# Kernel tuning notes

Measured on AMD Instinct MI355X. Metric: run time of the kernel, lower is better.

## Reference

```python
import jax, jax.numpy as jnp
import numpy as np

N = 262144      # number of 3D points
D = 128         # in_channels
NCLS = 20       # classes
M = 10          # num_prototype
EPS = 0.05      # sinkhorn epsilon
ITERS = 3       # sinkhorn iterations
GAMMA = 0.99    # EMA momentum
LN_EPS = 1e-5

def layer_norm(x, g, b):
    mu = jnp.mean(x, axis=-1, keepdims=True)
    v = jnp.mean((x - mu) ** 2, axis=-1, keepdims=True)
    return (x - mu) / jnp.sqrt(v + LN_EPS) * g + b

def l2n(x):
    # F.normalize(p=2, dim=-1) with eps=1e-12
    return x / jnp.clip(jnp.linalg.norm(x, axis=-1, keepdims=True), 1e-12)

def setup_inputs() -> dict:
    key = jax.random.key(0)
    k1, k2, k3 = jax.random.split(key, 3)
    return {
        "feature3d": jax.random.normal(k1, (N, D), dtype=jnp.float32),
        "gt_seg": jax.random.randint(k2, (N,), 0, NCLS, dtype=jnp.int32),
        "prototypes": jax.random.normal(k3, (NCLS, M, D), dtype=jnp.float32),
        "feat_gamma": jnp.ones((D,), jnp.float32),
        "feat_beta": jnp.zeros((D,), jnp.float32),
        "mask_gamma": jnp.ones((NCLS,), jnp.float32),
        "mask_beta": jnp.zeros((NCLS,), jnp.float32),
    }

def reference(feature3d, gt_seg, prototypes, feat_gamma, feat_beta, mask_gamma, mask_beta):
    _c = l2n(layer_norm(feature3d, feat_gamma, feat_beta))            # [N,D]
    protos = l2n(prototypes)                                          # [K,M,D]
    masks = jnp.einsum('nd,kmd->nmk', _c, protos)                     # [N,M,K]
    out_seg = layer_norm(jnp.max(masks, axis=1), mask_gamma, mask_beta)  # [N,K]

    # ---- prototype_learning ----
    pred = jnp.argmax(out_seg, axis=-1)
    correct = (gt_seg == pred).astype(_c.dtype)                       # [N]
    proto_logits = _c @ protos.reshape(-1, D).T                       # [N,K*M]

    sel = jax.nn.one_hot(gt_seg, NCLS, dtype=_c.dtype)                # [N,K]
    # masked per-class sinkhorn, vectorized across all 20 classes
    L = jnp.exp(jnp.transpose(masks, (2, 1, 0)) / EPS) * sel.T[:, None, :]  # [K,M,N]
    B = jnp.sum(sel, axis=0)                                          # [K] points per class
    s = jnp.sum(L, axis=(1, 2), keepdims=True)
    L = L / jnp.where(s > 0, s, 1.0)
    Bsafe = jnp.where(B > 0, B, 1.0)[:, None, None]
    for _ in range(ITERS):
        rs = jnp.sum(L, axis=2, keepdims=True)                        # per-prototype row sum
        L = L / (jnp.where(rs > 0, rs, 1.0) * M)
        cs = jnp.sum(L, axis=1, keepdims=True)                        # per-point col sum
        L = L / jnp.where(cs > 0, cs, 1.0) / Bsafe
    L = L * B[:, None, None]

    idx = jnp.argmax(L, axis=1)                                       # [K,N] hard assignment
    q = jax.nn.one_hot(idx, M, dtype=_c.dtype)                        # [K,N,M] (one_hot(argmax))

    w = sel.T * correct[None, :]                                      # [K,N] class-k AND correct
    m_q = q * w[:, :, None]                                           # [K,N,M]
    f = jnp.einsum('knm,nd->kmd', m_q, _c * correct[:, None])         # [K,M,D]
    ncount = jnp.sum(m_q, axis=1)                                     # [K,M]
    fn = l2n(f)
    upd = GAMMA * protos + (1.0 - GAMMA) * fn                         # momentum_update
    new_protos = l2n(jnp.where(ncount[..., None] > 0, upd, protos))   # [K,M,D]

    idx_pp = idx[gt_seg, jnp.arange(N)]                               # per-point proto index
    proto_target = (idx_pp + M * gt_seg).astype(jnp.float32)          # [N]
    return out_seg, proto_logits, proto_target, new_protos
```

## Files before the change

### kernel.cpp

```cpp
#include <hip/hip_runtime.h>
#include <hip/hip_bf16.h>

#define NPTS 262144
#define DIM  128
#define KC   20
#define MP   10
#define LNEPS 1e-5f
#define EPSI  0.05f
#define CCAP  65536

typedef _Float16 half8 __attribute__((ext_vector_type(8)));
typedef float f32x4 __attribute__((ext_vector_type(4)));
typedef float fv4 __attribute__((ext_vector_type(4)));

union H8U4 { half8 h; uint4 u; };

#define WS_PN     0
#define WS_PHI    25600
#define WS_PLO    39936
#define WS_F      54272
#define WS_NCOUNT 79872
#define WS_CCNT   80072
#define WS_UH     80080
#define WS_SK     80680
#define WS_BC     80700
#define WS_PSB    80720
#define WS_PR     244560
#define WS_EXPV   449360
#define WS_CIDX   3595088

#define EPIT 212

#define MFMA_(b_, a_, c_) __builtin_amdgcn_mfma_f32_16x16x32_f16(b_, a_, c_, 0, 0, 0)

__device__ __forceinline__ half8 lds_h8(const uint4* p) {
    return *reinterpret_cast<const half8*>(p);
}

__device__ __forceinline__ void gload_lds16(const uint4* g, uint4* l) {
    __builtin_amdgcn_global_load_lds(
        (const __attribute__((address_space(1))) void*)(g),
        (__attribute__((address_space(3))) void*)(l), 16, 0, 0);
}

__device__ __forceinline__ void nt_store4(float* p, float x, float y, float z, float w) {
    fv4 v = {x, y, z, w};
    __builtin_nontemporal_store(v, (fv4*)p);
}

__global__ __launch_bounds__(64) void k_norm_protos(
    const float* __restrict__ pr, float* __restrict__ pn,
    _Float16* __restrict__ phi, _Float16* __restrict__ plo)
{
    int j = blockIdx.x, l = threadIdx.x;
    const int jm = j & 15;
    const int s1 = l >> 3,       swz1 = (((s1 ^ jm) << 3) | (l & 7));
    const int s2 = 8 + (l >> 3), swz2 = (((s2 ^ jm) << 3) | (l & 7));
    if (j < 200) {
        float x0 = pr[(size_t)j*128 + l], x1 = pr[(size_t)j*128 + 64 + l];
        float ss = x0*x0 + x1*x1;
        #pragma unroll
        for (int off = 32; off > 0; off >>= 1) ss += __shfl_xor(ss, off);
        float dn = fmaxf(sqrtf(ss), 1e-12f);
        float y0 = x0/dn, y1 = x1/dn;
        pn[(size_t)j*128 + l]      = y0;
        pn[(size_t)j*128 + 64 + l] = y1;
        _Float16 h0 = (_Float16)y0, h1 = (_Float16)y1;
        phi[(size_t)j*128 + swz1] = h0;
        phi[(size_t)j*128 + swz2] = h1;
        plo[(size_t)j*128 + swz1] = (_Float16)(y0 - (float)h0);
        plo[(size_t)j*128 + swz2] = (_Float16)(y1 - (float)h1);
    } else {
        phi[(size_t)j*128 + swz1] = (_Float16)0.f;  phi[(size_t)j*128 + swz2] = (_Float16)0.f;
        plo[(size_t)j*128 + swz1] = (_Float16)0.f;  plo[(size_t)j*128 + swz2] = (_Float16)0.f;
    }
}

__global__ __launch_bounds__(256, 3) void k_main(
    const float* __restrict__ feat, const int* __restrict__ gt,
    const _Float16* __restrict__ phi, const _Float16* __restrict__ plo,
    const float* __restrict__ fg, const float* __restrict__ fb,
    const float* __restrict__ mg, const float* __restrict__ mb,
    float* __restrict__ out_seg, float* __restrict__ plog,
    float* __restrict__ expv, float* __restrict__ psb,
    int* __restrict__ cidx, int* __restrict__ ccnt)
{
    __shared__ __align__(16) char ldsb[33280];
    uint4* bbuf = (uint4*)ldsb;
    float* epi  = (float*)ldsb;
    float* osg  = (float*)(ldsb + 27136);
    float* exs  = (float*)(ldsb + 29696);
    float* sumS = (float*)(ldsb + 31232);
    int*   gtS  = (int*)  (ldsb + 31488);
    float* part = (float*)(ldsb + 31744);

    const int t = threadIdx.x, blk = blockIdx.x;
    const int w = t >> 6, lane = t & 63;
    const int l15 = lane & 15, l4 = lane >> 4;
    const int pbase = blk * 64;

    const uint4* phi4 = (const uint4*)phi;
    const uint4* plo4 = (const uint4*)plo;

#define STAGE_B(S, BI) do { \
        const uint4* gh = phi4 + (size_t)(S)*512 + t; \
        const uint4* gl = plo4 + (size_t)(S)*512 + t; \
        uint4* dh = bbuf + (BI)*1024 + w*64; \
        uint4* dl = bbuf + (BI)*1024 + 512 + w*64; \
        gload_lds16(gh,       dh); \
        gload_lds16(gh + 256, dh + 256); \
        gload_lds16(gl,       dl); \
        gload_lds16(gl + 256, dl + 256); \
    } while (0)

    STAGE_B(0, 0);

    const float4* gfeat = (const float4*)feat;
    float4 A[4][2];
    {
        size_t rb = (size_t)(pbase + w*16 + l15) * 32;
        #pragma unroll
        for (int kst = 0; kst < 4; ++kst)
            #pragma unroll
            for (int h = 0; h < 2; ++h)
                A[kst][h] = gfeat[rb + kst*8 + l4*2 + h];
    }
    float4 G[4][2], Bb[4][2];
    {
        const float4* fg4 = (const float4*)fg;
        const float4* fb4 = (const float4*)fb;
        #pragma unroll
        for (int kst = 0; kst < 4; ++kst)
            #pragma unroll
            for (int h = 0; h < 2; ++h) {
                G[kst][h]  = fg4[kst*8 + l4*2 + h];
                Bb[kst][h] = fb4[kst*8 + l4*2 + h];
            }
    }

    half8 fah[4], fal[4];
    {
        float s0 = 0.f;
        #pragma unroll
        for (int kst = 0; kst < 4; ++kst)
            #pragma unroll
            for (int h = 0; h < 2; ++h) {
                float4 v = A[kst][h];
                s0 += v.x + v.y + v.z + v.w;
            }
        s0 += __shfl_xor(s0, 16); s0 += __shfl_xor(s0, 32);
        float mean = s0 * (1.f/128.f);
        float s1 = 0.f;
        #pragma unroll
        for (int kst = 0; kst < 4; ++kst)
            #pragma unroll
            for (int h = 0; h < 2; ++h) {
                float4 v = A[kst][h];
                float a = v.x-mean, b = v.y-mean, c = v.z-mean, d = v.w-mean;
                s1 += a*a + b*b + c*c + d*d;
            }
        s1 += __shfl_xor(s1, 16); s1 += __shfl_xor(s1, 32);
        float rstd = rsqrtf(s1 * (1.f/128.f) + LNEPS);
        float s2 = 0.f;
        #pragma unroll
        for (int kst = 0; kst < 4; ++kst)
            #pragma unroll
            for (int h = 0; h < 2; ++h) {
                float4 v = A[kst][h];
                float4 g = G[kst][h], bb = Bb[kst][h];
                v.x = (v.x-mean)*rstd*g.x + bb.x;
                v.y = (v.y-mean)*rstd*g.y + bb.y;
                v.z = (v.z-mean)*rstd*g.z + bb.z;
                v.w = (v.w-mean)*rstd*g.w + bb.w;
                A[kst][h] = v;
                s2 += v.x*v.x + v.y*v.y + v.z*v.z + v.w*v.w;
            }
        s2 += __shfl_xor(s2, 16); s2 += __shfl_xor(s2, 32);
        float rl2 = 1.f / fmaxf(sqrtf(s2), 1e-12f);
        #pragma unroll
        for (int kst = 0; kst < 4; ++kst) {
            float4 va = A[kst][0], vb = A[kst][1];
            va.x*=rl2; va.y*=rl2; va.z*=rl2; va.w*=rl2;
            vb.x*=rl2; vb.y*=rl2; vb.z*=rl2; vb.w*=rl2;
            H8U4 h, lo;
            h.h[0]=(_Float16)va.x; h.h[1]=(_Float16)va.y; h.h[2]=(_Float16)va.z; h.h[3]=(_Float16)va.w;
            h.h[4]=(_Float16)vb.x; h.h[5]=(_Float16)vb.y; h.h[6]=(_Float16)vb.z; h.h[7]=(_Float16)vb.w;
            lo.h[0]=(_Float16)(va.x-(float)h.h[0]); lo.h[1]=(_Float16)(va.y-(float)h.h[1]);
            lo.h[2]=(_Float16)(va.z-(float)h.h[2]); lo.h[3]=(_Float16)(va.w-(float)h.h[3]);
            lo.h[4]=(_Float16)(vb.x-(float)h.h[4]); lo.h[5]=(_Float16)(vb.y-(float)h.h[5]);
            lo.h[6]=(_Float16)(vb.z-(float)h.h[6]); lo.h[7]=(_Float16)(vb.w-(float)h.h[7]);
            fah[kst] = h.h;
            fal[kst] = lo.h;
        }
    }

    f32x4 acc[13];
    #pragma unroll
    for (int nt = 0; nt < 13; ++nt)
        acc[nt] = (f32x4){0.f,0.f,0.f,0.f};

    __syncthreads();

    #pragma unroll
    for (int s = 0; s < 7; ++s) {
        if (s < 6) STAGE_B(s + 1, (s + 1) & 1);
        const uint4* bb = bbuf + (s & 1)*1024;
        if (s < 6) {
            #pragma unroll
            for (int kst = 0; kst < 4; ++kst) {
                const int slz = (kst*4 + l4) ^ l15;
                half8 b0h = lds_h8(bb + l15*16 + slz);
                half8 b0l = lds_h8(bb + 512 + l15*16 + slz);
                half8 b1h = lds_h8(bb + (16+l15)*16 + slz);
                half8 b1l = lds_h8(bb + 512 + (16+l15)*16 + slz);
                acc[2*s]   = MFMA_(b0h, fah[kst], acc[2*s]);
                acc[2*s+1] = MFMA_(b1h, fah[kst], acc[2*s+1]);
                acc[2*s]   = MFMA_(b0h, fal[kst], acc[2*s]);
                acc[2*s+1] = MFMA_(b1h, fal[kst], acc[2*s+1]);
                acc[2*s]   = MFMA_(b0l, fah[kst], acc[2*s]);
                acc[2*s+1] = MFMA_(b1l, fah[kst], acc[2*s+1]);
                acc[2*s]   = MFMA_(b0l, fal[kst], acc[2*s]);
                acc[2*s+1] = MFMA_(b1l, fal[kst], acc[2*s+1]);
            }
        } else {
            #pragma unroll
            for (int kst = 0; kst < 4; ++kst) {
                const int slz = (kst*4 + l4) ^ l15;
                half8 b0h = lds_h8(bb + l15*16 + slz);
                half8 b0l = lds_h8(bb + 512 + l15*16 + slz);
                acc[12] = MFMA_(b0h, fah[kst], acc[12]);
                acc[12] = MFMA_(b0h, fal[kst], acc[12]);
                acc[12] = MFMA_(b0l, fah[kst], acc[12]);
                acc[12] = MFMA_(b0l, fal[kst], acc[12]);
            }
        }
        __syncthreads();
    }

    #pragma unroll 1
    for (int p = 0; p < 2; ++p) {
        if ((w >> 1) == p) {
            int row = (w & 1)*16 + l15;
            #pragma unroll
            for (int nt = 0; nt < 13; ++nt)
                if (nt < 12 || l4 < 2) {
                    float4 sv;
                    sv.x = acc[nt][0]; sv.y = acc[nt][1];
                    sv.z = acc[nt][2]; sv.w = acc[nt][3];
                    *reinterpret_cast<float4*>(&epi[row*EPIT + nt*16 + l4*4]) = sv;
                }
        }
        __syncthreads();
        {
            float* pdst = plog + (size_t)(pbase + p*32)*200;
            #pragma unroll
            for (int it = 0; it < 7; ++it) {
                int f = it*256 + t;
                if (f < 1600) {
                    int row = f / 50, c4 = f - row*50;
                    const float* sp = &epi[row*EPIT + c4*4];
                    nt_store4(&pdst[(size_t)f*4], sp[0], sp[1], sp[2], sp[3]);
                }
            }
        }
        if (t < 128) {
            const int q = t >> 2, sub = t & 3;
            const int n = pbase + p*32 + q;
            float ml[5];
            #pragma unroll
            for (int kk = 0; kk < 5; ++kk) {
                int k = sub*5 + kk;
                float mx = epi[q*EPIT + k*10];
                #pragma unroll
                for (int m = 1; m < 10; ++m) mx = fmaxf(mx, epi[q*EPIT + k*10 + m]);
                ml[kk] = mx;
            }
            float s0 = ml[0]+ml[1]+ml[2]+ml[3]+ml[4];
            s0 += __shfl_xor(s0,1); s0 += __shfl_xor(s0,2);
            float mean = s0 / 20.f;
            float s1 = 0.f;
            #pragma unroll
            for (int kk = 0; kk < 5; ++kk) { float d = ml[kk]-mean; s1 += d*d; }
            s1 += __shfl_xor(s1,1); s1 += __shfl_xor(s1,2);
            float rstd = rsqrtf(s1 / 20.f + LNEPS);
            float bv = -1e30f; int bk = 0;
            #pragma unroll
            for (int kk = 0; kk < 5; ++kk) {
                int k = sub*5 + kk;
                float y = (ml[kk]-mean)*rstd*mg[k] + mb[k];
                osg[q*20 + k] = y;
                if (y > bv) { bv = y; bk = k; }
            }
            #pragma unroll
            for (int off = 1; off <= 2; off <<= 1) {
                float ov = __shfl_xor(bv, off);
                int   ok = __shfl_xor(bk, off);
                if (ov > bv || (ov == bv && ok < bk)) { bv = ov; bk = ok; }
            }
            int g = gt[n];
            if (sub == 0) {
                if (bk == g) {
                    int slot = atomicAdd(ccnt, 1);
                    if (slot < CCAP) cidx[slot] = n;
                }
                float se = 0.f;
                #pragma unroll
                for (int m = 0; m < 10; ++m) {
                    float e = expf(epi[q*EPIT + g*10 + m] / EPSI);
                    exs[q*12 + m] = e;
                    se += e;
                }
                exs[q*12 + 10] = 0.f;
                exs[q*12 + 11] = 0.f;
                sumS[p*32 + q] = se;
                gtS[p*32 + q]  = g;
            }
        }
        __syncthreads();
        if (t < 160) {
            const float* sp = &osg[t*4];
            nt_store4(&out_seg[(size_t)(pbase + p*32)*20 + t*4], sp[0], sp[1], sp[2], sp[3]);
        } else if (t < 256 && (t - 160) < 96)
            *reinterpret_cast<float4*>(&expv[(size_t)(pbase + p*32)*12 + (t-160)*4])
                = *reinterpret_cast<const float4*>(&exs[(t-160)*4]);
        __syncthreads();
    }

    if (t < 160) {
        int c = t >> 3, o = t & 7;
        float cnt = 0.f, sm = 0.f;
        for (int i = o*8; i < o*8 + 8; ++i)
            if (gtS[i] == c) { cnt += 1.f; sm += sumS[i]; }
        part[t] = cnt; part[160 + t] = sm;
    }
    __syncthreads();
    if (t < 20) {
        float cnt = 0.f, sm = 0.f;
        #pragma unroll
        for (int o = 0; o < 8; ++o) { cnt += part[t*8+o]; sm += part[160 + t*8+o]; }
        psb[(size_t)t*4096 + blk]      = cnt;
        psb[(size_t)(20+t)*4096 + blk] = sm;
    }
#undef STAGE_B
}

__global__ __launch_bounds__(256) void k_reduce_sB(
    const float* __restrict__ psb, float* __restrict__ sk, float* __restrict__ Bc)
{
    __shared__ float red[256];
    int t = threadIdx.x, rrow = blockIdx.x;
    float s = 0.f;
    #pragma unroll
    for (int i = 0; i < 16; ++i) s += psb[(size_t)rrow*4096 + i*256 + t];
    red[t] = s; __syncthreads();
    for (int off = 128; off > 0; off >>= 1) { if (t < off) red[t] += red[t+off]; __syncthreads(); }
    if (t == 0) { if (rrow < 20) Bc[rrow] = red[0]; else sk[rrow-20] = red[0]; }
}

__global__ __launch_bounds__(256) void k_row(int iter,
    const int* __restrict__ gt, const float* __restrict__ expv,
    const float* __restrict__ uh, const float* __restrict__ sk,
    const float* __restrict__ Bc, float* __restrict__ pr)
{
    __shared__ float prodS[2560];
    __shared__ int gtS[256];
    int t = threadIdx.x, b = blockIdx.x;
    int n = b*256 + t;
    int g = gt[n];
    float e[10];
    {
        const float4* e4 = (const float4*)(expv + (size_t)n*12);
        float4 ea = e4[0], eb = e4[1], ec = e4[2];
        e[0]=ea.x; e[1]=ea.y; e[2]=ea.z; e[3]=ea.w;
        e[4]=eb.x; e[5]=eb.y; e[6]=eb.z; e[7]=eb.w;
        e[8]=ec.x; e[9]=ec.y;
    }
    float skg = sk[g];
    float v = (skg > 0.f) ? 1.f/skg : 1.f;
    float B = Bc[g];
    float Bs = (B > 0.f) ? B : 1.f;
    for (int c = 1; c < iter; ++c) {
        const float* uc = uh + (c-1)*200 + g*10;
        float sc = 0.f;
        #pragma unroll
        for (int m = 0; m < 10; ++m) sc += e[m]*uc[m];
        v = (sc > 0.f) ? 1.f/(Bs*sc) : v/Bs;
    }
    #pragma unroll
    for (int m = 0; m < 10; ++m) prodS[t*10+m] = e[m]*v;
    gtS[t] = g;
    __syncthreads();
    if (t < 200) {
        int kk = t / 10, mm = t % 10;
        float acc = 0.f;
        for (int i = 0; i < 256; ++i)
            if (gtS[i] == kk) acc += prodS[i*10+mm];
        pr[(size_t)t*1024 + b] = acc;
    }
}

__global__ __launch_bounds__(256) void k_reduce_u(int iter,
    const float* __restrict__ pr, float* __restrict__ uh)
{
    __shared__ float red[256];
    int t = threadIdx.x, j = blockIdx.x;
    float s = 0.f;
    #pragma unroll
    for (int i = 0; i < 4; ++i) s += pr[(size_t)j*1024 + i*256 + t];
    red[t] = s; __syncthreads();
    for (int off = 128; off > 0; off >>= 1) { if (t < off) red[t] += red[t+off]; __syncthreads(); }
    if (t == 0) {
        float S = red[0];
        float uprev = (iter == 1) ? 1.f : uh[(iter-2)*200 + j];
        uh[(iter-1)*200 + j] = (S > 0.f) ? 1.f/(10.f*S) : uprev*0.1f;
    }
}

__global__ __launch_bounds__(256) void k_post(
    const int* __restrict__ gt, const float* __restrict__ expv,
    const float* __restrict__ u,
    const int* __restrict__ cidx, const int* __restrict__ ccnt,
    const float* __restrict__ feat, const float* __restrict__ fg,
    const float* __restrict__ fb,
    float* __restrict__ ptarget, float* __restrict__ facc,
    float* __restrict__ ncount)
{
    int t = threadIdx.x;
    {
        int n = blockIdx.x*256 + t;
        int g = gt[n];
        const float* uk = u + g*10;
        float bv = -1e30f; int idx = 0;
        #pragma unroll
        for (int m = 0; m < 10; ++m) {
            float pm = expv[(size_t)n*12 + m] * uk[m];
            if (pm > bv) { bv = pm; idx = m; }
        }
        ptarget[n] = (float)(idx + 10*g);
    }
    int wid = blockIdx.x*4 + (t >> 6);
    int lane = t & 63;
    int cnt = *ccnt; if (cnt > CCAP) cnt = CCAP;
    for (int i = wid; i < cnt; i += 4096) {
        int n = cidx[i];
        float x0 = feat[(size_t)n*128 + lane], x1 = feat[(size_t)n*128 + 64 + lane];
        float s = x0 + x1;
        #pragma unroll
        for (int off = 32; off > 0; off >>= 1) s += __shfl_xor(s, off);
        float mean = s * (1.f/128.f);
        float d0 = x0 - mean, d1 = x1 - mean;
        float s2 = d0*d0 + d1*d1;
        #pragma unroll
        for (int off = 32; off > 0; off >>= 1) s2 += __shfl_xor(s2, off);
        float rstd = rsqrtf(s2 * (1.f/128.f) + LNEPS);
        float y0 = d0*rstd*fg[lane] + fb[lane];
        float y1 = d1*rstd*fg[64+lane] + fb[64+lane];
        float s3 = y0*y0 + y1*y1;
        #pragma unroll
        for (int off = 32; off > 0; off >>= 1) s3 += __shfl_xor(s3, off);
        float rl2 = 1.f / fmaxf(sqrtf(s3), 1e-12f);
        float c0 = y0*rl2, c1 = y1*rl2;
        int g = gt[n];
        const float* uk = u + g*10;
        float bv = -1e30f; int idx = 0;
        #pragma unroll
        for (int m = 0; m < 10; ++m) {
            float pm = expv[(size_t)n*12 + m] * uk[m];
            if (pm > bv) { bv = pm; idx = m; }
        }
        float* frow = facc + (size_t)(g*10+idx)*128;
        atomicAdd(&frow[lane], c0);
        atomicAdd(&frow[64+lane], c1);
        if (lane == 0) atomicAdd(&ncount[g*10+idx], 1.f);
    }
}

__global__ __launch_bounds__(64) void k_proto_update(
    const float* __restrict__ facc, const float* __restrict__ ncount,
    const float* __restrict__ pn, float* __restrict__ outp)
{
    const float OMG = (float)(1.0 - 0.99);
    int j = blockIdx.x, l = threadIdx.x;
    float f0 = facc[(size_t)j*128+l], f1 = facc[(size_t)j*128+64+l];
    float ss = f0*f0 + f1*f1;
    #pragma unroll
    for (int off = 32; off > 0; off >>= 1) ss += __shfl_xor(ss, off);
    float fl2 = fmaxf(sqrtf(ss), 1e-12f);
    float fn0 = f0/fl2, fn1 = f1/fl2;
    float p0 = pn[(size_t)j*128+l], p1 = pn[(size_t)j*128+64+l];
    float u0 = 0.99f*p0 + OMG*fn0, u1 = 0.99f*p1 + OMG*fn1;
    bool ok = ncount[j] > 0.f;
    float s0 = ok ? u0 : p0, s1 = ok ? u1 : p1;
    float ss2 = s0*s0 + s1*s1;
    #pragma unroll
    for (int off = 32; off > 0; off >>= 1) ss2 += __shfl_xor(ss2, off);
    float l2 = fmaxf(sqrtf(ss2), 1e-12f);
    outp[(size_t)j*128+l]      = s0/l2;
    outp[(size_t)j*128+64+l]   = s1/l2;
}

extern "C" void kernel_launch(void* const* d_in, const int* in_sizes, int n_in,
                              void* d_out, int out_size, void* d_ws, size_t ws_size,
                              hipStream_t stream)
{
    const float* feat   = (const float*)d_in[0];
    const int*   gt     = (const int*)  d_in[1];
    const float* protos = (const float*)d_in[2];
    const float* fg     = (const float*)d_in[3];
    const float* fb     = (const float*)d_in[4];
    const float* mg     = (const float*)d_in[5];
    const float* mb     = (const float*)d_in[6];

    float* out      = (float*)d_out;
    float* out_seg  = out;
    float* plog     = out + (size_t)NPTS*20;
    float* ptarget  = out + (size_t)NPTS*220;
    float* newp     = out + (size_t)NPTS*221;

    float* ws   = (float*)d_ws;
    float* pn   = ws + WS_PN;
    _Float16* phi = (_Float16*)(ws + WS_PHI);
    _Float16* plo = (_Float16*)(ws + WS_PLO);
    float* facc = ws + WS_F;
    float* ncnt = ws + WS_NCOUNT;
    int*   ccnt = (int*)(ws + WS_CCNT);
    float* uh   = ws + WS_UH;
    float* sk   = ws + WS_SK;
    float* Bc   = ws + WS_BC;
    float* psb  = ws + WS_PSB;
    float* pr   = ws + WS_PR;
    float* expv = ws + WS_EXPV;
    int*   cidx = (int*)(ws + WS_CIDX);

    hipMemsetAsync(facc, 0, (25600 + 200 + 8)*sizeof(float), stream);
    hipLaunchKernelGGL(k_norm_protos, dim3(224), dim3(64), 0, stream, protos, pn, phi, plo);
    hipLaunchKernelGGL(k_main, dim3(4096), dim3(256), 0, stream,
                       feat, gt, phi, plo, fg, fb, mg, mb, out_seg, plog, expv, psb,
                       cidx, ccnt);
    hipLaunchKernelGGL(k_reduce_sB, dim3(40), dim3(256), 0, stream, psb, sk, Bc);
    for (int it = 1; it <= 3; ++it) {
        hipLaunchKernelGGL(k_row, dim3(1024), dim3(256), 0, stream, it, gt, expv, uh, sk, Bc, pr);
        hipLaunchKernelGGL(k_reduce_u, dim3(200), dim3(256), 0, stream, it, pr, uh);
    }
    hipLaunchKernelGGL(k_post, dim3(1024), dim3(256), 0, stream,
                       gt, expv, uh + 400, cidx, ccnt, feat, fg, fb, ptarget, facc, ncnt);
    hipLaunchKernelGGL(k_proto_update, dim3(200), dim3(64), 0, stream, facc, ncnt, pn, newp);
}
```

Before: 246.3 us.

## Fold first Sinkhorn row-sum pass into main kernel and pack exp values

The main kernel now accumulates per-block, per-(class,prototype) sums of the exp values and writes them as partials. A merged reduction kernel derives the point counts, the class sums and the first Sinkhorn row scaling directly from these partials, so the first k_row/k_reduce_u pass over all points is no longer launched. The exp buffer is also packed to 10 floats per point instead of 12 to cut bandwidth, and k_main's launch bound rises to 4 blocks per SIMD. In exchange the main kernel does extra LDS scans per block and writes a larger partial array, and the reduction kernel now runs serially over 11 rows per class.

```diff
diff --git a/kernel.cpp b/kernel.cpp
--- a/kernel.cpp
+++ b/kernel.cpp
@@ -25,9 +25,9 @@
 #define WS_SK     80680
 #define WS_BC     80700
 #define WS_PSB    80720
-#define WS_PR     244560
-#define WS_EXPV   449360
-#define WS_CIDX   3595088
+#define WS_EP     162640
+#define WS_EXPV   981840
+#define WS_CIDX   3603280
 
 #define EPIT 212
 
@@ -76,13 +76,13 @@
     }
 }
 
-__global__ __launch_bounds__(256, 3) void k_main(
+__global__ __launch_bounds__(256, 4) void k_main(
     const float* __restrict__ feat, const int* __restrict__ gt,
     const _Float16* __restrict__ phi, const _Float16* __restrict__ plo,
     const float* __restrict__ fg, const float* __restrict__ fb,
     const float* __restrict__ mg, const float* __restrict__ mb,
     float* __restrict__ out_seg, float* __restrict__ plog,
-    float* __restrict__ expv, float* __restrict__ psb,
+    float* __restrict__ expv, float* __restrict__ psb, float* __restrict__ ep,
     int* __restrict__ cidx, int* __restrict__ ccnt)
 {
     __shared__ __align__(16) char ldsb[33280];
@@ -90,9 +90,8 @@
     float* epi  = (float*)ldsb;
     float* osg  = (float*)(ldsb + 27136);
     float* exs  = (float*)(ldsb + 29696);
-    float* sumS = (float*)(ldsb + 31232);
-    int*   gtS  = (int*)  (ldsb + 31488);
-    float* part = (float*)(ldsb + 31744);
+    int*   gtS  = (int*)  (ldsb + 30976);
+    float* part = (float*)(ldsb + 31232);
 
     const int t = threadIdx.x, blk = blockIdx.x;
     const int w = t >> 6, lane = t & 63;
@@ -237,6 +236,7 @@
         __syncthreads();
     }
 
+    float eacc = 0.f;
     #pragma unroll 1
     for (int p = 0; p < 2; ++p) {
         if ((w >> 1) == p) {
@@ -303,58 +303,74 @@
                     int slot = atomicAdd(ccnt, 1);
                     if (slot < CCAP) cidx[slot] = n;
                 }
-                float se = 0.f;
                 #pragma unroll
-                for (int m = 0; m < 10; ++m) {
-                    float e = expf(epi[q*EPIT + g*10 + m] / EPSI);
-                    exs[q*12 + m] = e;
-                    se += e;
-                }
-                exs[q*12 + 10] = 0.f;
-                exs[q*12 + 11] = 0.f;
-                sumS[p*32 + q] = se;
-                gtS[p*32 + q]  = g;
+                for (int m = 0; m < 10; ++m)
+                    exs[q*10 + m] = expf(epi[q*EPIT + g*10 + m] / EPSI);
+                gtS[p*32 + q] = g;
             }
         }
         __syncthreads();
         if (t < 160) {
             const float* sp = &osg[t*4];
             nt_store4(&out_seg[(size_t)(pbase + p*32)*20 + t*4], sp[0], sp[1], sp[2], sp[3]);
-        } else if (t < 256 && (t - 160) < 96)
-            *reinterpret_cast<float4*>(&expv[(size_t)(pbase + p*32)*12 + (t-160)*4])
-                = *reinterpret_cast<const float4*>(&exs[(t-160)*4]);
+        } else if (t < 240) {
+            int f = t - 160;
+            *reinterpret_cast<float4*>(&expv[(size_t)(pbase + p*32)*10 + f*4])
+                = *reinterpret_cast<const float4*>(&exs[f*4]);
+        }
+        if (t < 200) {
+            int kk = t / 10, mm = t - kk*10;
+            #pragma unroll 4
+            for (int i = 0; i < 32; ++i)
+                if (gtS[p*32 + i] == kk) eacc += exs[i*10 + mm];
+        }
         __syncthreads();
     }
 
     if (t < 160) {
         int c = t >> 3, o = t & 7;
-        float cnt = 0.f, sm = 0.f;
+        float cnt = 0.f;
         for (int i = o*8; i < o*8 + 8; ++i)
-            if (gtS[i] == c) { cnt += 1.f; sm += sumS[i]; }
-        part[t] = cnt; part[160 + t] = sm;
+            if (gtS[i] == c) cnt += 1.f;
+        part[t] = cnt;
     }
     __syncthreads();
     if (t < 20) {
-        float cnt = 0.f, sm = 0.f;
-        #pragma unroll
-        for (int o = 0; o < 8; ++o) { cnt += part[t*8+o]; sm += part[160 + t*8+o]; }
-        psb[(size_t)t*4096 + blk]      = cnt;
-        psb[(size_t)(20+t)*4096 + blk] = sm;
-    }
+        float cnt = 0.f;
+        #pragma unroll
+        for (int o = 0; o < 8; ++o) cnt += part[t*8+o];
+        psb[(size_t)t*4096 + blk] = cnt;
+    }
+    if (t < 200) ep[(size_t)t*4096 + blk] = eacc;
 #undef STAGE_B
 }
 
-__global__ __launch_bounds__(256) void k_reduce_sB(
-    const float* __restrict__ psb, float* __restrict__ sk, float* __restrict__ Bc)
+__global__ __launch_bounds__(256) void k_red1(
+    const float* __restrict__ psb, const float* __restrict__ ep,
+    float* __restrict__ Bc, float* __restrict__ sk, float* __restrict__ uh)
 {
     __shared__ float red[256];
-    int t = threadIdx.x, rrow = blockIdx.x;
-    float s = 0.f;
-    #pragma unroll
-    for (int i = 0; i < 16; ++i) s += psb[(size_t)rrow*4096 + i*256 + t];
-    red[t] = s; __syncthreads();
-    for (int off = 128; off > 0; off >>= 1) { if (t < off) red[t] += red[t+off]; __syncthreads(); }
-    if (t == 0) { if (rrow < 20) Bc[rrow] = red[0]; else sk[rrow-20] = red[0]; }
+    __shared__ float rs[11];
+    int t = threadIdx.x, k = blockIdx.x;
+    for (int r = 0; r < 11; ++r) {
+        const float* src = (r == 0) ? (psb + (size_t)k*4096)
+                                    : (ep + (size_t)(k*10 + r - 1)*4096);
+        float s = 0.f;
+        #pragma unroll
+        for (int i = 0; i < 16; ++i) s += src[i*256 + t];
+        red[t] = s; __syncthreads();
+        for (int off = 128; off > 0; off >>= 1) { if (t < off) red[t] += red[t+off]; __syncthreads(); }
+        if (t == 0) rs[r] = red[0];
+        __syncthreads();
+    }
+    if (t < 16) {
+        float S = rs[1]+rs[2]+rs[3]+rs[4]+rs[5]+rs[6]+rs[7]+rs[8]+rs[9]+rs[10];
+        if (t == 0) { Bc[k] = rs[0]; sk[k] = S; }
+        if (t < 10) {
+            float r1 = (S > 0.f) ? rs[1+t] / S : rs[1+t];
+            uh[k*10 + t] = (r1 > 0.f) ? 1.f/(10.f*r1) : 0.1f;
+        }
+    }
 }
 
 __global__ __launch_bounds__(256) void k_row(int iter,
@@ -369,11 +385,10 @@
     int g = gt[n];
     float e[10];
     {
-        const float4* e4 = (const float4*)(expv + (size_t)n*12);
-        float4 ea = e4[0], eb = e4[1], ec = e4[2];
-        e[0]=ea.x; e[1]=ea.y; e[2]=ea.z; e[3]=ea.w;
-        e[4]=eb.x; e[5]=eb.y; e[6]=eb.z; e[7]=eb.w;
-        e[8]=ec.x; e[9]=ec.y;
+        const float2* e2 = (const float2*)(expv + (size_t)n*10);
+        float2 a0=e2[0], a1=e2[1], a2=e2[2], a3=e2[3], a4=e2[4];
+        e[0]=a0.x; e[1]=a0.y; e[2]=a1.x; e[3]=a1.y; e[4]=a2.x;
+        e[5]=a2.y; e[6]=a3.x; e[7]=a3.y; e[8]=a4.x; e[9]=a4.y;
     }
     float skg = sk[g];
     float v = (skg > 0.f) ? 1.f/skg : 1.f;
@@ -411,7 +426,7 @@
     for (int off = 128; off > 0; off >>= 1) { if (t < off) red[t] += red[t+off]; __syncthreads(); }
     if (t == 0) {
         float S = red[0];
-        float uprev = (iter == 1) ? 1.f : uh[(iter-2)*200 + j];
+        float uprev = uh[(iter-2)*200 + j];
         uh[(iter-1)*200 + j] = (S > 0.f) ? 1.f/(10.f*S) : uprev*0.1f;
     }
 }
@@ -430,11 +445,14 @@
         int n = blockIdx.x*256 + t;
         int g = gt[n];
         const float* uk = u + g*10;
+        const float2* e2 = (const float2*)(expv + (size_t)n*10);
         float bv = -1e30f; int idx = 0;
         #pragma unroll
-        for (int m = 0; m < 10; ++m) {
-            float pm = expv[(size_t)n*12 + m] * uk[m];
-            if (pm > bv) { bv = pm; idx = m; }
+        for (int m2 = 0; m2 < 5; ++m2) {
+            float2 ev = e2[m2];
+            float p0 = ev.x * uk[m2*2], p1 = ev.y * uk[m2*2+1];
+            if (p0 > bv) { bv = p0; idx = m2*2; }
+            if (p1 > bv) { bv = p1; idx = m2*2+1; }
         }
         ptarget[n] = (float)(idx + 10*g);
     }
@@ -462,11 +480,14 @@
         float c0 = y0*rl2, c1 = y1*rl2;
         int g = gt[n];
         const float* uk = u + g*10;
+        const float2* e2 = (const float2*)(expv + (size_t)n*10);
         float bv = -1e30f; int idx = 0;
         #pragma unroll
-        for (int m = 0; m < 10; ++m) {
-            float pm = expv[(size_t)n*12 + m] * uk[m];
-            if (pm > bv) { bv = pm; idx = m; }
+        for (int m2 = 0; m2 < 5; ++m2) {
+            float2 ev = e2[m2];
+            float p0 = ev.x * uk[m2*2], p1 = ev.y * uk[m2*2+1];
+            if (p0 > bv) { bv = p0; idx = m2*2; }
+            if (p1 > bv) { bv = p1; idx = m2*2+1; }
         }
         float* frow = facc + (size_t)(g*10+idx)*128;
         atomicAdd(&frow[lane], c0);
@@ -528,17 +549,18 @@
     float* sk   = ws + WS_SK;
     float* Bc   = ws + WS_BC;
     float* psb  = ws + WS_PSB;
-    float* pr   = ws + WS_PR;
+    float* ep   = ws + WS_EP;
+    float* pr   = ws + WS_EP;
     float* expv = ws + WS_EXPV;
     int*   cidx = (int*)(ws + WS_CIDX);
 
     hipMemsetAsync(facc, 0, (25600 + 200 + 8)*sizeof(float), stream);
     hipLaunchKernelGGL(k_norm_protos, dim3(224), dim3(64), 0, stream, protos, pn, phi, plo);
     hipLaunchKernelGGL(k_main, dim3(4096), dim3(256), 0, stream,
-                       feat, gt, phi, plo, fg, fb, mg, mb, out_seg, plog, expv, psb,
+                       feat, gt, phi, plo, fg, fb, mg, mb, out_seg, plog, expv, psb, ep,
                        cidx, ccnt);
-    hipLaunchKernelGGL(k_reduce_sB, dim3(40), dim3(256), 0, stream, psb, sk, Bc);
-    for (int it = 1; it <= 3; ++it) {
+    hipLaunchKernelGGL(k_red1, dim3(20), dim3(256), 0, stream, psb, ep, Bc, sk, uh);
+    for (int it = 2; it <= 3; ++it) {
         hipLaunchKernelGGL(k_row, dim3(1024), dim3(256), 0, stream, it, gt, expv, uh, sk, Bc, pr);
         hipLaunchKernelGGL(k_reduce_u, dim3(200), dim3(256), 0, stream, it, pr, uh);
     }
```

New measurement: 242.1 us. No clear change (-1.7%).
